# Performance work log

Hardware: AMD Instinct MI355X
Metric: run time of the kernel (lower is better)

Reference implementation:

```python
import jax, jax.numpy as jnp
import numpy as np

N = 20000   # nodes
E = 320000  # directed edges (before self-loops)
D = 64      # input_dim
H = 10      # GAT heads
HD = H * D  # 640
NEG_SLOPE = 0.2


def setup_inputs() -> dict:
    key = jax.random.key(0)
    ks = jax.random.split(key, 10)
    return {
        "x": jax.random.normal(ks[0], (N, D), jnp.float32),
        "W_gat": jax.random.normal(ks[1], (D, HD), jnp.float32) / np.sqrt(D).astype(np.float32),
        "att_src": jax.random.normal(ks[2], (H, D), jnp.float32) / np.sqrt(D).astype(np.float32),
        "att_dst": jax.random.normal(ks[3], (H, D), jnp.float32) / np.sqrt(D).astype(np.float32),
        "b_gat": jnp.zeros((HD,), jnp.float32),
        "W_gcn": jax.random.normal(ks[4], (HD, HD), jnp.float32) / np.sqrt(HD).astype(np.float32),
        "b_gcn": jnp.zeros((HD,), jnp.float32),
        "W1": jax.random.normal(ks[5], (2 * HD, 1500), jnp.float32) / np.sqrt(2 * HD).astype(np.float32),
        "b1": jnp.zeros((1500,), jnp.float32),
        "W2": jax.random.normal(ks[6], (1500, 10), jnp.float32) / np.sqrt(1500).astype(np.float32),
        "b2": jnp.zeros((10,), jnp.float32),
        "edge_index": jax.random.randint(ks[7], (2, E), 0, N, dtype=jnp.int64),
    }


def _forward(x, W_gat, att_src, att_dst, b_gat, W_gcn, b_gcn, W1, b1, W2, b2, edge_index):
    n = x.shape[0]
    # add self-loops (PyG default for both GATConv and GCNConv)
    loop = jnp.arange(n, dtype=edge_index.dtype)
    ei = jnp.concatenate([edge_index, jnp.stack([loop, loop])], axis=1)
    src, dst = ei[0], ei[1]

    # ---- GATConv(D -> D, heads=H, concat) ----
    xl = (x @ W_gat).reshape(n, H, D)                      # [N,H,D]
    a_src = jnp.einsum('nhd,hd->nh', xl, att_src)          # [N,H]
    a_dst = jnp.einsum('nhd,hd->nh', xl, att_dst)          # [N,H]
    alpha = jax.nn.leaky_relu(a_src[src] + a_dst[dst], NEG_SLOPE)  # [E',H]
    m = jax.ops.segment_max(alpha, dst, num_segments=n)    # segment softmax over incoming edges
    ex = jnp.exp(alpha - m[dst])
    den = jax.ops.segment_sum(ex, dst, num_segments=n)
    w = ex / (den[dst] + 1e-16)                            # [E',H]
    msg = xl[src] * w[:, :, None]                          # [E',H,D]
    x1 = jax.ops.segment_sum(msg, dst, num_segments=n).reshape(n, HD) + b_gat
    x1 = jax.nn.relu(x1)

    # ---- GCNConv(HD -> HD), symmetric norm with self-loops ----
    deg = jax.ops.segment_sum(jnp.ones(ei.shape[1], x.dtype), dst, num_segments=n)
    dinv = jnp.where(deg > 0, jax.lax.rsqrt(deg), 0.0)
    norm = dinv[src] * dinv[dst]                           # [E']
    xw = x1 @ W_gcn                                        # [N,HD]
    x2 = jax.ops.segment_sum(xw[src] * norm[:, None], dst, num_segments=n) + b_gcn
    x2 = jax.nn.relu(x2)

    # ---- global max/mean pool (batch=None -> single graph) + MLP head ----
    pooled = jnp.concatenate([x2.max(axis=0, keepdims=True),
                              x2.mean(axis=0, keepdims=True)], axis=1)  # [1, 2*HD]
    h = jax.nn.relu(pooled @ W1 + b1)
    # dropout is identity in eval mode
    return h @ W2 + b2                                     # [1, 10]


def reference(x, W_gat, att_src, att_dst, b_gat, W_gcn, b_gcn, W1, b1, W2, b2, edge_index):
    return _forward(x, W_gat, att_src, att_dst, b_gat, W_gcn, b_gcn, W1, b1, W2, b2, edge_index)
```

## Files before the change

kernel.cpp:

```cpp
#include <hip/hip_runtime.h>
#include <hip/hip_bf16.h>
#include <math.h>

#define NN 20000
#define DD 64
#define HH 10
#define HDIM 640
#define NEG 0.2f
#define H1 1500
#define BKK 64

typedef _Float16 half8 __attribute__((ext_vector_type(8)));
typedef _Float16 half4v __attribute__((ext_vector_type(4)));
typedef float f32x4 __attribute__((ext_vector_type(4)));

__global__ __launch_bounds__(256) void k_cvtB(const float* __restrict__ Wgcn,
                                              const float* __restrict__ Wg,
                                              _Float16* __restrict__ Wbt,
                                              _Float16* __restrict__ WgT)
{
    __shared__ float t[32][33];
    const int bx = blockIdx.x;
    int by = blockIdx.y;
    const float* W; _Float16* WT; int rows, cols;
    if (by < 20) { W = Wgcn; WT = Wbt; rows = HDIM; cols = HDIM; }
    else         { W = Wg;   WT = WgT; rows = DD;   cols = HDIM; by -= 20; }
    const int lx = threadIdx.x & 31, ly = threadIdx.x >> 5;
    #pragma unroll
    for (int i = ly; i < 32; i += 8)
        t[i][lx] = W[(size_t)(by * 32 + i) * cols + bx * 32 + lx];
    __syncthreads();
    #pragma unroll
    for (int j = ly; j < 32; j += 8)
        WT[(size_t)(bx * 32 + j) * rows + by * 32 + lx] = (_Float16)t[lx][j];
}

__global__ __launch_bounds__(256) void k_gemm1(
    const float* __restrict__ x, const _Float16* __restrict__ WgT,
    const float* __restrict__ att_s, const float* __restrict__ att_d,
    _Float16* __restrict__ xl, float* __restrict__ aST, float* __restrict__ aDT)
{
    __shared__ _Float16 As[128][72];
    __shared__ _Float16 Bs[64][72];
    const int tid = threadIdx.x;
    const int m0 = blockIdx.x * 128;
    const int h  = blockIdx.y;
    const int n0 = h * 64;

    {
        const int row = tid >> 1, ch = (tid & 1) * 32;
        const int gr = m0 + row;
        if (gr < NN) {
            const float* xp = &x[(size_t)gr * DD + ch];
            #pragma unroll
            for (int i = 0; i < 8; ++i) {
                const float4 v = *(const float4*)&xp[i * 4];
                half4v o = {(_Float16)v.x, (_Float16)v.y, (_Float16)v.z, (_Float16)v.w};
                *(half4v*)&As[row][ch + i * 4] = o;
            }
        } else {
            const half8 z = {0, 0, 0, 0, 0, 0, 0, 0};
            #pragma unroll
            for (int i = 0; i < 4; ++i) *(half8*)&As[row][ch + i * 8] = z;
        }
    }
    {
        const int row = tid >> 2, part = (tid & 3) * 16;
        const _Float16* wp = &WgT[(size_t)(n0 + row) * DD + part];
        *(half8*)&Bs[row][part]     = *(const half8*)&wp[0];
        *(half8*)&Bs[row][part + 8] = *(const half8*)&wp[8];
    }
    __syncthreads();

    const int lane = tid & 63, wave = tid >> 6;
    const int l15 = lane & 15, quad = lane >> 4;
    f32x4 acc[2][4];
    #pragma unroll
    for (int r = 0; r < 2; ++r)
        #pragma unroll
        for (int c = 0; c < 4; ++c) acc[r][c] = (f32x4){0.f, 0.f, 0.f, 0.f};

    #pragma unroll
    for (int ks = 0; ks < 2; ++ks) {
        const half8 a0 = *(const half8*)&As[wave * 32 + l15][ks * 32 + quad * 8];
        const half8 a1 = *(const half8*)&As[wave * 32 + 16 + l15][ks * 32 + quad * 8];
        #pragma unroll
        for (int c = 0; c < 4; ++c) {
            const half8 b = *(const half8*)&Bs[c * 16 + l15][ks * 32 + quad * 8];
            acc[0][c] = __builtin_amdgcn_mfma_f32_16x16x32_f16(a0, b, acc[0][c], 0, 0, 0);
            acc[1][c] = __builtin_amdgcn_mfma_f32_16x16x32_f16(a1, b, acc[1][c], 0, 0, 0);
        }
    }

    float asv[4], adv[4];
    #pragma unroll
    for (int c = 0; c < 4; ++c) {
        asv[c] = att_s[h * DD + c * 16 + l15];
        adv[c] = att_d[h * DD + c * 16 + l15];
    }
    #pragma unroll
    for (int r = 0; r < 2; ++r) {
        float ps[4] = {0.f, 0.f, 0.f, 0.f}, pd[4] = {0.f, 0.f, 0.f, 0.f};
        #pragma unroll
        for (int c = 0; c < 4; ++c)
            #pragma unroll
            for (int g = 0; g < 4; ++g) {
                ps[g] = fmaf(acc[r][c][g], asv[c], ps[g]);
                pd[g] = fmaf(acc[r][c][g], adv[c], pd[g]);
            }
        #pragma unroll
        for (int m = 1; m <= 8; m <<= 1)
            #pragma unroll
            for (int g = 0; g < 4; ++g) {
                ps[g] += __shfl_xor(ps[g], m);
                pd[g] += __shfl_xor(pd[g], m);
            }
        #pragma unroll
        for (int c = 0; c < 4; ++c)
            #pragma unroll
            for (int g = 0; g < 4; ++g) {
                const int row = m0 + wave * 32 + r * 16 + quad * 4 + g;
                if (row < NN)
                    xl[(size_t)row * HDIM + n0 + c * 16 + l15] = (_Float16)acc[r][c][g];
            }
        if (l15 == 0)
            #pragma unroll
            for (int g = 0; g < 4; ++g) {
                const int row = m0 + wave * 32 + r * 16 + quad * 4 + g;
                if (row < NN) {
                    aST[(size_t)h * NN + row] = ps[g];
                    aDT[(size_t)h * NN + row] = pd[g];
                }
            }
    }
}

__global__ void k_count(const int* __restrict__ ei, int E, int* __restrict__ cnt)
{
    const int e = blockIdx.x * blockDim.x + threadIdx.x;
    if (e >= E + NN) return;
    const int d = (e < E) ? ei[E + e] : (e - E);
    atomicAdd(&cnt[d], 1);
}

__global__ __launch_bounds__(1024) void k_scan(const int* __restrict__ cnt,
                                               int* __restrict__ rowptr,
                                               float* __restrict__ dinv)
{
    __shared__ int sh[1024];
    const int t = threadIdx.x;
    const int CH = 20;
    const int base = t * CH;
    int loc[CH];
    int s = 0;
    #pragma unroll
    for (int i = 0; i < CH; ++i) {
        const int idx = base + i;
        const int c = (idx < NN) ? cnt[idx] : 0;
        loc[i] = s; s += c;
    }
    sh[t] = s; __syncthreads();
    for (int off = 1; off < 1024; off <<= 1) {
        const int v = (t >= off) ? sh[t - off] : 0;
        __syncthreads();
        sh[t] += v;
        __syncthreads();
    }
    const int prev = (t == 0) ? 0 : sh[t - 1];
    #pragma unroll
    for (int i = 0; i < CH; ++i) {
        const int idx = base + i;
        if (idx < NN) {
            rowptr[idx] = prev + loc[i];
            dinv[idx]   = rsqrtf((float)cnt[idx]);
        }
    }
    if (t == 1023) rowptr[NN] = sh[1023];
}

__global__ void k_fill(const int* __restrict__ ei, int E,
                       const int* __restrict__ rowptr,
                       int* __restrict__ cursor, int* __restrict__ csr)
{
    const int e = blockIdx.x * blockDim.x + threadIdx.x;
    if (e >= E + NN) return;
    int s, d;
    if (e < E) { s = ei[e]; d = ei[E + e]; } else { s = d = e - E; }
    const int pos = atomicAdd(&cursor[d], 1);
    csr[rowptr[d] + pos] = s;
}

__device__ __forceinline__ bool slice_map3(int bid, int& s, int& m)
{
    const int r = bid & 7, k = bid >> 3;
    if (k < 625) { s = r; m = k; return true; }
    s = 8 + (r >> 2);
    m = (r & 3) * 157 + (k - 625);
    return m < 625;
}

__device__ __forceinline__ float lrexp(float a)
{
    a = (a >= 0.f) ? a : NEG * a;
    return __expf(a);
}

__global__ __launch_bounds__(256) void k_gat_gather4(
    const int* __restrict__ rowptr, const int* __restrict__ csr,
    const float* __restrict__ aST, const float* __restrict__ aDT,
    const _Float16* __restrict__ xl, const float* __restrict__ b_gat,
    _Float16* __restrict__ x1)
{
    int s, m;
    if (!slice_map3(blockIdx.x, s, m)) return;
    const int wave = threadIdx.x >> 6, lane = threadIdx.x & 63;
    const int g = lane >> 3, l = lane & 7;
    const int n = m * 32 + wave * 8 + g;
    const int col = s * 64 + l * 8;
    const float* __restrict__ as = aST + (size_t)s * NN;
    const _Float16* __restrict__ xc = xl + col;
    const float ad = aDT[(size_t)s * NN + n];

    float acc[8];
    #pragma unroll
    for (int i = 0; i < 8; ++i) acc[i] = 0.f;
    float ws = 0.f;

    const int j0 = rowptr[n], j1 = rowptr[n + 1];
    int j = j0;
    for (; j + 3 < j1; j += 4) {
        const int sA = csr[j], sB = csr[j + 1], sC = csr[j + 2], sD = csr[j + 3];
        const float wA = lrexp(as[sA] + ad);
        const float wB = lrexp(as[sB] + ad);
        const float wC = lrexp(as[sC] + ad);
        const float wD = lrexp(as[sD] + ad);
        ws += wA + wB + wC + wD;
        const half8 vA = *(const half8*)&xc[(size_t)sA * HDIM];
        const half8 vB = *(const half8*)&xc[(size_t)sB * HDIM];
        const half8 vC = *(const half8*)&xc[(size_t)sC * HDIM];
        const half8 vD = *(const half8*)&xc[(size_t)sD * HDIM];
        #pragma unroll
        for (int i = 0; i < 8; ++i) {
            acc[i] = fmaf(wA, (float)vA[i], acc[i]);
            acc[i] = fmaf(wB, (float)vB[i], acc[i]);
            acc[i] = fmaf(wC, (float)vC[i], acc[i]);
            acc[i] = fmaf(wD, (float)vD[i], acc[i]);
        }
    }
    for (; j < j1; ++j) {
        const int sA = csr[j];
        const float wA = lrexp(as[sA] + ad);
        ws += wA;
        const half8 vA = *(const half8*)&xc[(size_t)sA * HDIM];
        #pragma unroll
        for (int i = 0; i < 8; ++i) acc[i] = fmaf(wA, (float)vA[i], acc[i]);
    }

    const float rr = 1.f / (ws + 1e-16f);
    const float4 ba = *(const float4*)&b_gat[col];
    const float4 bb = *(const float4*)&b_gat[col + 4];
    const float bv[8] = {ba.x, ba.y, ba.z, ba.w, bb.x, bb.y, bb.z, bb.w};
    half8 o;
    #pragma unroll
    for (int i = 0; i < 8; ++i) {
        const float v = fmaf(acc[i], rr, bv[i]);
        o[i] = (_Float16)((v > 0.f) ? v : 0.f);
    }
    *(half8*)&x1[(size_t)n * HDIM + col] = o;
}

__global__ __launch_bounds__(256) void k_gcn_gather4(
    const int* __restrict__ rowptr, const int* __restrict__ csr,
    const float* __restrict__ dinv, const _Float16* __restrict__ x1,
    _Float16* __restrict__ t)
{
    int s, m;
    if (!slice_map3(blockIdx.x, s, m)) return;
    const int wave = threadIdx.x >> 6, lane = threadIdx.x & 63;
    const int g = lane >> 3, l = lane & 7;
    const int n = m * 32 + wave * 8 + g;
    const int col = s * 64 + l * 8;
    const _Float16* __restrict__ xc = x1 + col;
    const float dd = dinv[n];

    float acc[8];
    #pragma unroll
    for (int i = 0; i < 8; ++i) acc[i] = 0.f;

    const int j0 = rowptr[n], j1 = rowptr[n + 1];
    int j = j0;
    for (; j + 3 < j1; j += 4) {
        const int sA = csr[j], sB = csr[j + 1], sC = csr[j + 2], sD = csr[j + 3];
        const float wA = dinv[sA], wB = dinv[sB];
        const float wC = dinv[sC], wD = dinv[sD];
        const half8 vA = *(const half8*)&xc[(size_t)sA * HDIM];
        const half8 vB = *(const half8*)&xc[(size_t)sB * HDIM];
        const half8 vC = *(const half8*)&xc[(size_t)sC * HDIM];
        const half8 vD = *(const half8*)&xc[(size_t)sD * HDIM];
        #pragma unroll
        for (int i = 0; i < 8; ++i) {
            acc[i] = fmaf(wA, (float)vA[i], acc[i]);
            acc[i] = fmaf(wB, (float)vB[i], acc[i]);
            acc[i] = fmaf(wC, (float)vC[i], acc[i]);
            acc[i] = fmaf(wD, (float)vD[i], acc[i]);
        }
    }
    for (; j < j1; ++j) {
        const int sA = csr[j];
        const float wA = dinv[sA];
        const half8 vA = *(const half8*)&xc[(size_t)sA * HDIM];
        #pragma unroll
        for (int i = 0; i < 8; ++i) acc[i] = fmaf(wA, (float)vA[i], acc[i]);
    }

    half8 o;
    #pragma unroll
    for (int i = 0; i < 8; ++i) o[i] = (_Float16)(acc[i] * dd);
    *(half8*)&t[(size_t)n * HDIM + col] = o;
}

__global__ __launch_bounds__(256) void k_gemm2(const _Float16* __restrict__ X,
                                               const _Float16* __restrict__ Wbt,
                                               const float* __restrict__ b_gcn,
                                               float* __restrict__ pmax,
                                               float* __restrict__ psum)
{
    __shared__ _Float16 Bs[2][128 * BKK];
    const int bid = blockIdx.x;
    const int r = bid & 7, q = bid >> 3;
    const int strip = (q / 5) * 8 + r;
    const int nt = q % 5;
    if (strip >= 157) return;

    const int tid = threadIdx.x;
    const int lane = tid & 63, wave = tid >> 6;
    const int l15 = lane & 15, quad = lane >> 4;
    const int m0 = strip * 128 + wave * 32;
    const int n0 = nt * 128;

    f32x4 acc[2][8];
    #pragma unroll
    for (int rr = 0; rr < 2; ++rr)
        #pragma unroll
        for (int c = 0; c < 8; ++c) acc[rr][c] = (f32x4){0.f, 0.f, 0.f, 0.f};

    const _Float16* a0p = &X[(size_t)(m0 + l15) * HDIM + quad * 8];
    const _Float16* a1p = a0p + (size_t)16 * HDIM;
    const int srow = wave * 8 + (lane >> 3);
    const int sck  = lane & 7;

#define STAGE4(buf, kb)                                                          \
    {                                                                            \
        _Pragma("unroll")                                                        \
        for (int i = 0; i < 4; ++i) {                                            \
            const int rw = i * 32 + srow;                                        \
            const int ck = sck ^ (rw & 7);                                       \
            const _Float16* src = &Wbt[(size_t)(n0 + rw) * HDIM + (kb) + ck * 8];\
            __builtin_amdgcn_global_load_lds(                                    \
                (const __attribute__((address_space(1))) void*)src,              \
                (__attribute__((address_space(3))) void*)&Bs[buf][((size_t)i * 256 + tid) * 8], \
                16, 0, 0);                                                       \
        }                                                                        \
    }

    STAGE4(0, 0);
    for (int it = 0; it < 10; ++it) {
        const int kb = it * BKK;
        half8 a0[2], a1[2];
        #pragma unroll
        for (int ks = 0; ks < 2; ++ks) {
            a0[ks] = *(const half8*)(a0p + kb + ks * 32);
            a1[ks] = *(const half8*)(a1p + kb + ks * 32);
        }
        if (it < 9) {
            STAGE4((it + 1) & 1, kb + BKK);
            asm volatile("s_waitcnt vmcnt(4)" ::: "memory");
        } else {
            asm volatile("s_waitcnt vmcnt(0)" ::: "memory");
        }
        __builtin_amdgcn_s_barrier();
        __builtin_amdgcn_sched_barrier(0);
        const _Float16* Bsc = Bs[it & 1];
        #pragma unroll
        for (int ks = 0; ks < 2; ++ks) {
            #pragma unroll
            for (int c = 0; c < 8; ++c) {
                const int br = c * 16 + l15;
                const int ck = (ks * 4 + quad) ^ (br & 7);
                const half8 b = *(const half8*)&Bsc[(size_t)br * BKK + ck * 8];
                acc[0][c] = __builtin_amdgcn_mfma_f32_16x16x32_f16(a0[ks], b, acc[0][c], 0, 0, 0);
                acc[1][c] = __builtin_amdgcn_mfma_f32_16x16x32_f16(a1[ks], b, acc[1][c], 0, 0, 0);
            }
        }
        __builtin_amdgcn_sched_barrier(0);
        __builtin_amdgcn_s_barrier();
        __builtin_amdgcn_sched_barrier(0);
    }
#undef STAGE4

    float lmax[8], lsum[8];
    #pragma unroll
    for (int c = 0; c < 8; ++c) { lmax[c] = 0.f; lsum[c] = 0.f; }
    #pragma unroll
    for (int c = 0; c < 8; ++c) {
        const float bb = b_gcn[n0 + c * 16 + l15];
        #pragma unroll
        for (int rr = 0; rr < 2; ++rr)
            #pragma unroll
            for (int g = 0; g < 4; ++g) {
                const int row = m0 + rr * 16 + quad * 4 + g;
                if (row < NN) {
                    float v = acc[rr][c][g] + bb;
                    v = (v > 0.f) ? v : 0.f;
                    lmax[c] = fmaxf(lmax[c], v);
                    lsum[c] += v;
                }
            }
    }
    float* redm = (float*)Bs;
    float* reds = redm + 128;
    if (tid < 128) { redm[tid] = 0.f; reds[tid] = 0.f; }
    __syncthreads();
    #pragma unroll
    for (int c = 0; c < 8; ++c) {
        const int col = c * 16 + l15;
        atomicMax((int*)&redm[col], __float_as_int(lmax[c]));
        atomicAdd(&reds[col], lsum[c]);
    }
    __syncthreads();
    if (tid < 128) {
        atomicMax((int*)&pmax[n0 + tid], __float_as_int(redm[tid]));
        atomicAdd(&psum[n0 + tid], reds[tid]);
    }
}

__global__ __launch_bounds__(256) void k_mlp1(const float* __restrict__ pmax,
                                              const float* __restrict__ psum,
                                              const float* __restrict__ W1,
                                              float* __restrict__ hacc)
{
    __shared__ float pl[80];
    const int t = threadIdx.x;
    const int i0 = blockIdx.y * 80;
    if (t < 80) {
        const int i = i0 + t;
        pl[t] = (i < HDIM) ? pmax[i] : psum[i - HDIM] * (1.0f / NN);
    }
    __syncthreads();
    const int j = blockIdx.x * 256 + t;
    if (j >= H1) return;
    float acc = 0.f;
    #pragma unroll 8
    for (int i = 0; i < 80; ++i)
        acc = fmaf(pl[i], W1[(size_t)(i0 + i) * H1 + j], acc);
    atomicAdd(&hacc[j], acc);
}

__global__ __launch_bounds__(256) void k_mlp2(const float* __restrict__ hacc,
                                              const float* __restrict__ b1,
                                              const float* __restrict__ W2,
                                              const float* __restrict__ b2,
                                              float* __restrict__ out)
{
    __shared__ float hsh[H1];
    __shared__ float red[256];
    const int t = threadIdx.x;
    for (int i = t; i < H1; i += 256) {
        const float v = hacc[i] + b1[i];
        hsh[i] = (v > 0.f) ? v : 0.f;
    }
    __syncthreads();
    float acc[10];
    #pragma unroll
    for (int k = 0; k < 10; ++k) acc[k] = 0.f;
    for (int i = t; i < H1; i += 256) {
        const float h = hsh[i];
        #pragma unroll
        for (int k = 0; k < 10; ++k) acc[k] = fmaf(h, W2[i * 10 + k], acc[k]);
    }
    for (int k = 0; k < 10; ++k) {
        red[t] = acc[k]; __syncthreads();
        for (int s2 = 128; s2 > 0; s2 >>= 1) {
            if (t < s2) red[t] += red[t + s2];
            __syncthreads();
        }
        if (t == 0) out[k] = red[0] + b2[k];
        __syncthreads();
    }
}

extern "C" void kernel_launch(void* const* d_in, const int* in_sizes, int n_in,
                              void* d_out, int out_size, void* d_ws, size_t ws_size,
                              hipStream_t stream)
{
    const float* x     = (const float*)d_in[0];
    const float* Wg    = (const float*)d_in[1];
    const float* att_s = (const float*)d_in[2];
    const float* att_d = (const float*)d_in[3];
    const float* b_gat = (const float*)d_in[4];
    const float* Wgcn  = (const float*)d_in[5];
    const float* b_gcn = (const float*)d_in[6];
    const float* W1    = (const float*)d_in[7];
    const float* b1    = (const float*)d_in[8];
    const float* W2    = (const float*)d_in[9];
    const float* b2    = (const float*)d_in[10];
    const int*   ei    = (const int*)d_in[11];
    const int E = in_sizes[11] / 2;
    const int EP = E + NN;
    float* out = (float*)d_out;

    char* wsp = (char*)d_ws;
    size_t off = 0;
    auto alc = [&](size_t b) { void* p = wsp + off; off += (b + 255) & ~(size_t)255; return p; };
    _Float16* bufA = (_Float16*)alc((size_t)NN * HDIM * 2);
    _Float16* bufB = (_Float16*)alc((size_t)NN * HDIM * 2);
    float* aST    = (float*)alc((size_t)HH * NN * 4);
    float* aDT    = (float*)alc((size_t)HH * NN * 4);
    int*   rowptr = (int*)alc((size_t)(NN + 1) * 4);
    int*   csr    = (int*)alc((size_t)EP * 4);
    float* dinv   = (float*)alc((size_t)NN * 4);
    _Float16* Wbt = (_Float16*)alc((size_t)HDIM * HDIM * 2);
    _Float16* WgT = (_Float16*)alc((size_t)HDIM * DD * 2);
    const size_t zoff = off;
    int*   cnt    = (int*)alc((size_t)NN * 4);
    int*   cursor = (int*)alc((size_t)NN * 4);
    float* pmax   = (float*)alc((size_t)HDIM * 4);
    float* psum   = (float*)alc((size_t)HDIM * 4);
    float* hacc   = (float*)alc((size_t)H1 * 4);
    const size_t zsize = off - zoff;

    hipMemsetAsync(cnt, 0, zsize, stream);

    dim3 gw(HDIM / 32, HDIM / 32 + DD / 32);
    k_cvtB<<<gw, 256, 0, stream>>>(Wgcn, Wg, Wbt, WgT);
    dim3 g1((NN + 127) / 128, HH);
    k_gemm1<<<g1, 256, 0, stream>>>(x, WgT, att_s, att_d, bufA, aST, aDT);
    k_count<<<(EP + 255) / 256, 256, 0, stream>>>(ei, E, cnt);
    k_scan<<<1, 1024, 0, stream>>>(cnt, rowptr, dinv);
    k_fill<<<(EP + 255) / 256, 256, 0, stream>>>(ei, E, rowptr, cursor, csr);
    const int GG = 6256;
    k_gat_gather4<<<GG, 256, 0, stream>>>(rowptr, csr, aST, aDT, bufA, b_gat, bufB);
    k_gcn_gather4<<<GG, 256, 0, stream>>>(rowptr, csr, dinv, bufB, bufA);
    k_gemm2<<<800, 256, 0, stream>>>(bufA, Wbt, b_gcn, pmax, psum);
    dim3 gm1(6, 16);
    k_mlp1<<<gm1, 256, 0, stream>>>(pmax, psum, W1, hacc);
    k_mlp2<<<1, 256, 0, stream>>>(hacc, b1, W2, b2, out);
}
```

Measured before the change: 321.3 us.

## Merge independent kernels into combined launches to cut launch count

```diff
diff --git a/kernel.cpp b/kernel.cpp
--- a/kernel.cpp
+++ b/kernel.cpp
@@ -14,37 +14,95 @@
 typedef _Float16 half4v __attribute__((ext_vector_type(4)));
 typedef float f32x4 __attribute__((ext_vector_type(4)));
 
-__global__ __launch_bounds__(256) void k_cvtB(const float* __restrict__ Wgcn,
+__global__ __launch_bounds__(256) void k_prep(const float* __restrict__ Wgcn,
                                               const float* __restrict__ Wg,
                                               _Float16* __restrict__ Wbt,
-                                              _Float16* __restrict__ WgT)
-{
-    __shared__ float t[32][33];
-    const int bx = blockIdx.x;
-    int by = blockIdx.y;
-    const float* W; _Float16* WT; int rows, cols;
-    if (by < 20) { W = Wgcn; WT = Wbt; rows = HDIM; cols = HDIM; }
-    else         { W = Wg;   WT = WgT; rows = DD;   cols = HDIM; by -= 20; }
-    const int lx = threadIdx.x & 31, ly = threadIdx.x >> 5;
-    #pragma unroll
-    for (int i = ly; i < 32; i += 8)
-        t[i][lx] = W[(size_t)(by * 32 + i) * cols + bx * 32 + lx];
-    __syncthreads();
-    #pragma unroll
-    for (int j = ly; j < 32; j += 8)
-        WT[(size_t)(bx * 32 + j) * rows + by * 32 + lx] = (_Float16)t[lx][j];
-}
-
-__global__ __launch_bounds__(256) void k_gemm1(
+                                              _Float16* __restrict__ WgT,
+                                              const int* __restrict__ ei, int E,
+                                              int* __restrict__ cnt)
+{
+    const int bid = blockIdx.x;
+    if (bid < 440) {
+        __shared__ float t[32][33];
+        const int bx = bid % 20;
+        int by = bid / 20;
+        const float* W; _Float16* WT; int rows, cols;
+        if (by < 20) { W = Wgcn; WT = Wbt; rows = HDIM; cols = HDIM; }
+        else         { W = Wg;   WT = WgT; rows = DD;   cols = HDIM; by -= 20; }
+        const int lx = threadIdx.x & 31, ly = threadIdx.x >> 5;
+        #pragma unroll
+        for (int i = ly; i < 32; i += 8)
+            t[i][lx] = W[(size_t)(by * 32 + i) * cols + bx * 32 + lx];
+        __syncthreads();
+        #pragma unroll
+        for (int j = ly; j < 32; j += 8)
+            WT[(size_t)(bx * 32 + j) * rows + by * 32 + lx] = (_Float16)t[lx][j];
+    } else {
+        const int e = (bid - 440) * 256 + threadIdx.x;
+        if (e >= E + NN) return;
+        const int d = (e < E) ? ei[E + e] : (e - E);
+        atomicAdd(&cnt[d], 1);
+    }
+}
+
+__global__ __launch_bounds__(1024) void k_scan(const int* __restrict__ cnt,
+                                               int* __restrict__ rowptr,
+                                               float* __restrict__ dinv)
+{
+    __shared__ int sh[1024];
+    const int t = threadIdx.x;
+    const int CH = 20;
+    const int base = t * CH;
+    int loc[CH];
+    int s = 0;
+    #pragma unroll
+    for (int i = 0; i < CH; ++i) {
+        const int idx = base + i;
+        const int c = (idx < NN) ? cnt[idx] : 0;
+        loc[i] = s; s += c;
+    }
+    sh[t] = s; __syncthreads();
+    for (int off = 1; off < 1024; off <<= 1) {
+        const int v = (t >= off) ? sh[t - off] : 0;
+        __syncthreads();
+        sh[t] += v;
+        __syncthreads();
+    }
+    const int prev = (t == 0) ? 0 : sh[t - 1];
+    #pragma unroll
+    for (int i = 0; i < CH; ++i) {
+        const int idx = base + i;
+        if (idx < NN) {
+            rowptr[idx] = prev + loc[i];
+            dinv[idx]   = rsqrtf((float)cnt[idx]);
+        }
+    }
+    if (t == 1023) rowptr[NN] = sh[1023];
+}
+
+__global__ __launch_bounds__(256) void k_big(
     const float* __restrict__ x, const _Float16* __restrict__ WgT,
     const float* __restrict__ att_s, const float* __restrict__ att_d,
-    _Float16* __restrict__ xl, float* __restrict__ aST, float* __restrict__ aDT)
-{
+    _Float16* __restrict__ xl, float* __restrict__ aST, float* __restrict__ aDT,
+    const int* __restrict__ ei, int E, const int* __restrict__ rowptr,
+    int* __restrict__ cursor, int* __restrict__ csr)
+{
+    const int bid = blockIdx.x;
+    if (bid >= 1570) {
+        const int e = (bid - 1570) * 256 + threadIdx.x;
+        if (e >= E + NN) return;
+        int s, d;
+        if (e < E) { s = ei[e]; d = ei[E + e]; } else { s = d = e - E; }
+        const int pos = atomicAdd(&cursor[d], 1);
+        csr[rowptr[d] + pos] = s;
+        return;
+    }
+
     __shared__ _Float16 As[128][72];
     __shared__ _Float16 Bs[64][72];
     const int tid = threadIdx.x;
-    const int m0 = blockIdx.x * 128;
-    const int h  = blockIdx.y;
+    const int m0 = (bid % 157) * 128;
+    const int h  = bid / 157;
     const int n0 = h * 64;
 
     {
@@ -133,61 +191,6 @@
                 }
             }
     }
-}
-
-__global__ void k_count(const int* __restrict__ ei, int E, int* __restrict__ cnt)
-{
-    const int e = blockIdx.x * blockDim.x + threadIdx.x;
-    if (e >= E + NN) return;
-    const int d = (e < E) ? ei[E + e] : (e - E);
-    atomicAdd(&cnt[d], 1);
-}
-
-__global__ __launch_bounds__(1024) void k_scan(const int* __restrict__ cnt,
-                                               int* __restrict__ rowptr,
-                                               float* __restrict__ dinv)
-{
-    __shared__ int sh[1024];
-    const int t = threadIdx.x;
-    const int CH = 20;
-    const int base = t * CH;
-    int loc[CH];
-    int s = 0;
-    #pragma unroll
-    for (int i = 0; i < CH; ++i) {
-        const int idx = base + i;
-        const int c = (idx < NN) ? cnt[idx] : 0;
-        loc[i] = s; s += c;
-    }
-    sh[t] = s; __syncthreads();
-    for (int off = 1; off < 1024; off <<= 1) {
-        const int v = (t >= off) ? sh[t - off] : 0;
-        __syncthreads();
-        sh[t] += v;
-        __syncthreads();
-    }
-    const int prev = (t == 0) ? 0 : sh[t - 1];
-    #pragma unroll
-    for (int i = 0; i < CH; ++i) {
-        const int idx = base + i;
-        if (idx < NN) {
-            rowptr[idx] = prev + loc[i];
-            dinv[idx]   = rsqrtf((float)cnt[idx]);
-        }
-    }
-    if (t == 1023) rowptr[NN] = sh[1023];
-}
-
-__global__ void k_fill(const int* __restrict__ ei, int E,
-                       const int* __restrict__ rowptr,
-                       int* __restrict__ cursor, int* __restrict__ csr)
-{
-    const int e = blockIdx.x * blockDim.x + threadIdx.x;
-    if (e >= E + NN) return;
-    int s, d;
-    if (e < E) { s = ei[e]; d = ei[E + e]; } else { s = d = e - E; }
-    const int pos = atomicAdd(&cursor[d], 1);
-    csr[rowptr[d] + pos] = s;
 }
 
 __device__ __forceinline__ bool slice_map3(int bid, int& s, int& m)
@@ -434,12 +437,18 @@
     }
 }
 
-__global__ __launch_bounds__(256) void k_mlp1(const float* __restrict__ pmax,
-                                              const float* __restrict__ psum,
-                                              const float* __restrict__ W1,
-                                              float* __restrict__ hacc)
+__global__ __launch_bounds__(256) void k_mlp(const float* __restrict__ pmax,
+                                             const float* __restrict__ psum,
+                                             const float* __restrict__ W1,
+                                             const float* __restrict__ b1,
+                                             const float* __restrict__ W2,
+                                             const float* __restrict__ b2,
+                                             float* __restrict__ hacc,
+                                             int* __restrict__ done,
+                                             float* __restrict__ out)
 {
     __shared__ float pl[80];
+    __shared__ int isLast;
     const int t = threadIdx.x;
     const int i0 = blockIdx.y * 80;
     if (t < 80) {
@@ -448,25 +457,26 @@
     }
     __syncthreads();
     const int j = blockIdx.x * 256 + t;
-    if (j >= H1) return;
-    float acc = 0.f;
-    #pragma unroll 8
-    for (int i = 0; i < 80; ++i)
-        acc = fmaf(pl[i], W1[(size_t)(i0 + i) * H1 + j], acc);
-    atomicAdd(&hacc[j], acc);
-}
-
-__global__ __launch_bounds__(256) void k_mlp2(const float* __restrict__ hacc,
-                                              const float* __restrict__ b1,
-                                              const float* __restrict__ W2,
-                                              const float* __restrict__ b2,
-                                              float* __restrict__ out)
-{
+    if (j < H1) {
+        float acc = 0.f;
+        #pragma unroll 8
+        for (int i = 0; i < 80; ++i)
+            acc = fmaf(pl[i], W1[(size_t)(i0 + i) * H1 + j], acc);
+        atomicAdd(&hacc[j], acc);
+    }
+    __threadfence();
+    __syncthreads();
+    if (t == 0) {
+        const int total = gridDim.x * gridDim.y;
+        isLast = (atomicAdd(done, 1) == total - 1) ? 1 : 0;
+    }
+    __syncthreads();
+    if (!isLast) return;
+
     __shared__ float hsh[H1];
     __shared__ float red[256];
-    const int t = threadIdx.x;
     for (int i = t; i < H1; i += 256) {
-        const float v = hacc[i] + b1[i];
+        const float v = atomicAdd(&hacc[i], 0.0f) + b1[i];
         hsh[i] = (v > 0.f) ? v : 0.f;
     }
     __syncthreads();
@@ -527,22 +537,20 @@
     float* pmax   = (float*)alc((size_t)HDIM * 4);
     float* psum   = (float*)alc((size_t)HDIM * 4);
     float* hacc   = (float*)alc((size_t)H1 * 4);
+    int*   done   = (int*)alc(256);
     const size_t zsize = off - zoff;
 
     hipMemsetAsync(cnt, 0, zsize, stream);
 
-    dim3 gw(HDIM / 32, HDIM / 32 + DD / 32);
-    k_cvtB<<<gw, 256, 0, stream>>>(Wgcn, Wg, Wbt, WgT);
-    dim3 g1((NN + 127) / 128, HH);
-    k_gemm1<<<g1, 256, 0, stream>>>(x, WgT, att_s, att_d, bufA, aST, aDT);
-    k_count<<<(EP + 255) / 256, 256, 0, stream>>>(ei, E, cnt);
+    const int CNTB = (EP + 255) / 256;
+    k_prep<<<440 + CNTB, 256, 0, stream>>>(Wgcn, Wg, Wbt, WgT, ei, E, cnt);
     k_scan<<<1, 1024, 0, stream>>>(cnt, rowptr, dinv);
-    k_fill<<<(EP + 255) / 256, 256, 0, stream>>>(ei, E, rowptr, cursor, csr);
+    k_big<<<1570 + CNTB, 256, 0, stream>>>(x, WgT, att_s, att_d, bufA, aST, aDT,
+                                           ei, E, rowptr, cursor, csr);
     const int GG = 6256;
     k_gat_gather4<<<GG, 256, 0, stream>>>(rowptr, csr, aST, aDT, bufA, b_gat, bufB);
     k_gcn_gather4<<<GG, 256, 0, stream>>>(rowptr, csr, dinv, bufB, bufA);
     k_gemm2<<<800, 256, 0, stream>>>(bufA, Wbt, b_gcn, pmax, psum);
-    dim3 gm1(6, 16);
-    k_mlp1<<<gm1, 256, 0, stream>>>(pmax, psum, W1, hacc);
-    k_mlp2<<<1, 256, 0, stream>>>(hacc, b1, W2, b2, out);
-}
+    dim3 gm(6, 16);
+    k_mlp<<<gm, 256, 0, stream>>>(pmax, psum, W1, b1, W2, b2, hacc, done, out);
+}
```

Measured after the change: 318.3 us (median of 2 runs). About the same (-0.9%).
